# Performance work log

Hardware: AMD Instinct MI355X
Metric: run time of the kernel (lower is better)

The kernel has to match this reference:

```python
import jax, jax.numpy as jnp
import numpy as np

KH, KW = 3, 3
STRIDE = (1, 1)
PAD = (1, 1)
DIL = (1, 1)
DG = 1  # num_deformable_groups


def _out_size(h, pad, dil, k, stride):
    return (h + 2 * pad - (dil * (k - 1) + 1)) // stride + 1


def setup_inputs() -> dict:
    key = jax.random.key(0)
    k1, k2, k3 = jax.random.split(key, 3)
    B, Cin, H, W = 8, 128, 64, 64
    Cout = 128
    Ho = _out_size(H, PAD[0], DIL[0], KH, STRIDE[0])
    Wo = _out_size(W, PAD[1], DIL[1], KW, STRIDE[1])
    x = jax.random.normal(k1, (B, Cin, H, W), jnp.float32)
    offset = jax.random.normal(k2, (B, 2 * DG * KH * KW, Ho, Wo), jnp.float32)
    n = Cin * KH * KW
    stdv = 1.0 / np.sqrt(n)
    weight = jax.random.uniform(k3, (Cout, Cin, KH, KW), jnp.float32, -stdv, stdv)
    return {"x": x, "offset": offset, "weight": weight}


def deform_conv2d(x, offset, weight):
    B, Cin, H, W = x.shape
    Cout, _, kh, kw = weight.shape
    K = kh * kw
    Ho = _out_size(H, PAD[0], DIL[0], kh, STRIDE[0])
    Wo = _out_size(W, PAD[1], DIL[1], kw, STRIDE[1])
    G = DG
    Cg = Cin // G

    # base sampling grid per kernel tap: [kh,kw,Ho,Wo]
    by = (jnp.arange(kh) * DIL[0])[:, None, None, None] + (jnp.arange(Ho) * STRIDE[0] - PAD[0])[None, None, :, None]
    bx = (jnp.arange(kw) * DIL[1])[None, :, None, None] + (jnp.arange(Wo) * STRIDE[1] - PAD[1])[None, None, None, :]
    by = jnp.broadcast_to(by, (kh, kw, Ho, Wo)).reshape(K, Ho, Wo).astype(x.dtype)
    bx = jnp.broadcast_to(bx, (kh, kw, Ho, Wo)).reshape(K, Ho, Wo).astype(x.dtype)

    # offset layout: channel = g*2*K + 2*k + {0: dy, 1: dx}
    off = offset.reshape(B, G, K, 2, Ho, Wo)
    py = by[None, None] + off[:, :, :, 0]  # [B,G,K,Ho,Wo]
    px = bx[None, None] + off[:, :, :, 1]

    y0 = jnp.floor(py).astype(jnp.int32)
    x0 = jnp.floor(px).astype(jnp.int32)
    wy = (py - y0).reshape(B, G, 1, -1)  # fractional parts, [B,G,1,K*Ho*Wo]
    wx = (px - x0).reshape(B, G, 1, -1)

    xg = x.reshape(B, G, Cg, H * W)
    N = K * Ho * Wo

    def gather(yi, xi):
        valid = ((yi >= 0) & (yi < H) & (xi >= 0) & (xi < W)).reshape(B, G, 1, N)
        idx = (jnp.clip(yi, 0, H - 1) * W + jnp.clip(xi, 0, W - 1)).reshape(B, G, 1, N)
        v = jnp.take_along_axis(xg, jnp.broadcast_to(idx, (B, G, Cg, N)), axis=3)
        return v * valid.astype(x.dtype)

    v00 = gather(y0, x0)
    v01 = gather(y0, x0 + 1)
    v10 = gather(y0 + 1, x0)
    v11 = gather(y0 + 1, x0 + 1)

    cols = (v00 * (1 - wy) * (1 - wx) + v01 * (1 - wy) * wx
            + v10 * wy * (1 - wx) + v11 * wy * wx)
    cols = cols.reshape(B, G, Cg, K, Ho, Wo)  # deformable im2col columns

    wr = weight.reshape(Cout, G, Cg, K)
    return jnp.einsum('ogck,bgcknm->bonm', wr, cols)


def reference(x, offset, weight):
    return deform_conv2d(x, offset, weight)
```

## Files before the change

### kernel.cpp

```cpp
#include <hip/hip_runtime.h>
#include <hip/hip_fp16.h>

typedef __attribute__((ext_vector_type(4))) float f32x4;
typedef __attribute__((ext_vector_type(8))) _Float16 f16x8;
typedef __attribute__((ext_vector_type(4))) unsigned int u32x4;

__device__ __forceinline__ unsigned short f2h(float f) {
  __half h = __float2half_rn(f);
  unsigned short u;
  __builtin_memcpy(&u, &h, 2);
  return u;
}
__device__ __forceinline__ __half2 h2_of(unsigned int u) {
  __half2 h;
  __builtin_memcpy(&h, &u, 4);
  return h;
}
__device__ __forceinline__ unsigned int u_of(__half2 h) {
  unsigned int u;
  __builtin_memcpy(&u, &h, 4);
  return u;
}

__global__ __launch_bounds__(256) void xtrans_kernel(const float* __restrict__ x,
                                                     unsigned short* __restrict__ xt) {
  int t = blockIdx.x * 256 + threadIdx.x;
  int p  = t & 4095;
  int cg = (t >> 12) & 15;
  int b  = t >> 16;
  const float* xp = x + (((size_t)(b * 128 + cg * 8)) << 12) + p;
  unsigned int r[8];
#pragma unroll
  for (int j = 0; j < 8; ++j) r[j] = f2h(xp[(size_t)j << 12]);
  u32x4 pk;
  pk.x = r[0] | (r[1] << 16);
  pk.y = r[2] | (r[3] << 16);
  pk.z = r[4] | (r[5] << 16);
  pk.w = r[6] | (r[7] << 16);
  *reinterpret_cast<u32x4*>(xt + ((((size_t)b << 12) + p) << 7) + cg * 8) = pk;
}

__global__ __launch_bounds__(256) void wtrans_kernel(const float* __restrict__ w,
                                                     unsigned short* __restrict__ wf) {
  int tid = blockIdx.x * 256 + threadIdx.x;
  int l  = tid & 63;
  int mt = (tid >> 6) & 7;
  int ch = tid >> 9;
  int cc = ch / 9, tap = ch - cc * 9;
  int co = mt * 16 + (l & 15);
  int cb = cc * 32 + (l >> 4) * 8;
  unsigned int r[8];
#pragma unroll
  for (int j = 0; j < 8; ++j)
    r[j] = f2h(w[(co * 128 + cb + j) * 9 + tap]);
  u32x4 pk;
  pk.x = r[0] | (r[1] << 16);
  pk.y = r[2] | (r[3] << 16);
  pk.z = r[4] | (r[5] << 16);
  pk.w = r[6] | (r[7] << 16);
  *reinterpret_cast<u32x4*>(wf + (size_t)tid * 8) = pk;
}

__global__ __launch_bounds__(512, 1) void deform_kernel(const unsigned short* __restrict__ xt,
                                                        const float* __restrict__ off,
                                                        const unsigned short* __restrict__ wf,
                                                        float* __restrict__ out) {
  __shared__ __align__(16) unsigned char sWin[137216];
  __shared__ int   sPos[1152];
  __shared__ uint2 sWt[1152];

  const int tid = threadIdx.x;
  const int bid = blockIdx.x;
  const int b   = bid & 7;
  const int ho0 = (bid >> 3) * 2;
  const int r0  = min(max(ho0 - 3, 0), 56);

  for (int r = tid; r < 1152; r += 512) {
    int row = (r >= 576) ? 1 : 0;
    int rr  = r - row * 576;
    int tap = rr >> 6, wo = rr & 63;
    int ho = ho0 + row;
    float dy = off[((b * 18 + 2 * tap)     * 64 + ho) * 64 + wo];
    float dx = off[((b * 18 + 2 * tap + 1) * 64 + ho) * 64 + wo];
    float py = (float)(ho + (tap / 3) - 1) + dy;
    float px = (float)(wo + (tap % 3) - 1) + dx;
    float fy = floorf(py), fx = floorf(px);
    int y0 = (int)fy, x0 = (int)fx;
    float wy = py - fy, wx = px - fx;
    float wt = (y0 >= 0 && y0 < 64) ? (1.f - wy) : 0.f;
    float wb = (y0 + 1 >= 0 && y0 + 1 < 64) ? wy : 0.f;
    int y0c = min(max(y0, 0), 63), y1c = min(max(y0 + 1, 0), 63);
    int bx; float wl, wr;
    if (x0 >= 0 && x0 <= 62)      { bx = x0; wl = 1.f - wx; wr = wx;       }
    else if (x0 == -1)            { bx = 0;  wl = wx;       wr = 0.f;      }
    else if (x0 == 63)            { bx = 62; wl = 0.f;      wr = 1.f - wx; }
    else                          { bx = 0;  wl = 0.f;      wr = 0.f;      }
    sPos[r] = (y0c * 64 + bx) | ((y1c != y0c) ? (1 << 15) : 0);
    __half2 tp = __floats2half2_rn(wt * wl, wt * wr);
    __half2 bp = __floats2half2_rn(wb * wl, wb * wr);
    uint2 ww;
    ww.x = u_of(tp);
    ww.y = u_of(bp);
    sWt[r] = ww;
  }

  {
    const unsigned short* xrow = xt + ((size_t)b << 19) + ((size_t)r0 << 13);
#pragma unroll
    for (int it = 0; it < 16; ++it) {
      int idx = it * 512 + tid;
      int c = idx & 15;
      int p = (idx >> 4) & 63;
      int r = idx >> 10;
      u32x4 v;
      __builtin_memcpy(&v, xrow + (((size_t)(r * 64 + p)) << 7) + c * 8, 16);
      *reinterpret_cast<u32x4*>(&sWin[r * 16384 + p * 256 + (((c + p) & 15) << 4)]) = v;
    }
  }
  __syncthreads();

  const int l   = tid & 63;
  const int w   = tid >> 6;
  const int ks  = w & 3;
  const int row = w >> 2;
  const int ln  = l & 15;
  const int kg  = l >> 4;
  const int c16 = ks * 4 + kg;
  const int ho  = ho0 + row;

  const unsigned short* xtb = xt + ((size_t)b << 19) + ks * 32 + kg * 8;
  const unsigned short* wfb = wf + (size_t)l * 8;

  f32x4 acc[4][8] = {};

  for (int tap = 0; tap < 9; ++tap) {
    const int ch = ks * 9 + tap;

    f16x8 A[8];
    const unsigned short* wp = wfb + (size_t)(ch * 8) * 512;
#pragma unroll
    for (int mt = 0; mt < 8; ++mt)
      A[mt] = *reinterpret_cast<const f16x8*>(wp + (size_t)mt * 512);

#pragma unroll
    for (int pg = 0; pg < 4; ++pg) {
      const int e = row * 576 + tap * 64 + pg * 16 + ln;
      const int   pp = sPos[e];
      const uint2 ww = sWt[e];

      const int aX = pp & 4095;
      const int aY = aX + ((pp >> 9) & 64);
      const int tx  = aX & 63;
      const int twr = (aX >> 6) - r0;
      const int bwr = (aY >> 6) - r0;
      const bool tin = (unsigned)twr < 8u;
      const bool bin = (unsigned)bwr < 8u;

      u32x4 T0, T1, B0, B1;
      {
        int cT0 = ((c16 + tx) & 15) << 4, cT1 = ((c16 + tx + 1) & 15) << 4;
        int baseT = (tin ? twr : 0) * 16384 + tx * 256;
        __builtin_memcpy(&T0, &sWin[baseT + cT0],       16);
        __builtin_memcpy(&T1, &sWin[baseT + 256 + cT1], 16);
        int baseB = (bin ? bwr : 0) * 16384 + tx * 256;
        __builtin_memcpy(&B0, &sWin[baseB + cT0],       16);
        __builtin_memcpy(&B1, &sWin[baseB + 256 + cT1], 16);
      }
      if (!tin) {
        const unsigned short* p0 = xtb + ((size_t)aX << 7);
        __builtin_memcpy(&T0, p0,       16);
        __builtin_memcpy(&T1, p0 + 128, 16);
      }
      if (!bin) {
        const unsigned short* p1 = xtb + ((size_t)aY << 7);
        __builtin_memcpy(&B0, p1,       16);
        __builtin_memcpy(&B1, p1 + 128, 16);
      }

      const __half2 wtl = __half2half2(__low2half(h2_of(ww.x)));
      const __half2 wtr = __half2half2(__high2half(h2_of(ww.x)));
      const __half2 wbl = __half2half2(__low2half(h2_of(ww.y)));
      const __half2 wbr = __half2half2(__high2half(h2_of(ww.y)));
      u32x4 pk;
#pragma unroll
      for (int d = 0; d < 4; ++d) {
        __half2 s = __hmul2(wtl, h2_of(T0[d]));
        s = __hfma2(wtr, h2_of(T1[d]), s);
        s = __hfma2(wbl, h2_of(B0[d]), s);
        s = __hfma2(wbr, h2_of(B1[d]), s);
        pk[d] = u_of(s);
      }
      f16x8 bfrag;
      __builtin_memcpy(&bfrag, &pk, 16);

#pragma unroll
      for (int mt = 0; mt < 8; ++mt)
        acc[pg][mt] = __builtin_amdgcn_mfma_f32_16x16x32_f16(A[mt], bfrag,
                                                             acc[pg][mt], 0, 0, 0);
    }
  }

  float* sF = reinterpret_cast<float*>(sWin);
#define WR_LDS                                                                 \
  { _Pragma("unroll") for (int pg = 0; pg < 4; ++pg)                           \
    _Pragma("unroll") for (int mt = 0; mt < 8; ++mt)                           \
      *reinterpret_cast<f32x4*>(&sF[row * 8448 + (pg * 16 + ln) * 132 + mt * 16 + kg * 4]) = acc[pg][mt]; }
#define RD_LDS                                                                 \
  { _Pragma("unroll") for (int pg = 0; pg < 4; ++pg)                           \
    _Pragma("unroll") for (int mt = 0; mt < 8; ++mt) {                         \
      f32x4 v = *reinterpret_cast<const f32x4*>(&sF[row * 8448 + (pg * 16 + ln) * 132 + mt * 16 + kg * 4]); \
      acc[pg][mt] += v; } }

  __syncthreads();
  if (ks == 1) WR_LDS
  __syncthreads();
  if (ks == 0) RD_LDS
  __syncthreads();
  if (ks == 3) WR_LDS
  __syncthreads();
  if (ks == 2) RD_LDS
  __syncthreads();
  if (ks == 2) WR_LDS
  __syncthreads();
  if (ks == 0) RD_LDS
#undef WR_LDS
#undef RD_LDS

  {
    const int b2 = 16896 + row * 8704;
    if (ks == 0) {
#pragma unroll
      for (int pg = 0; pg < 4; ++pg)
#pragma unroll
        for (int mt = 0; mt < 8; ++mt)
#pragma unroll
          for (int rg = 0; rg < 4; ++rg)
            sF[b2 + (mt * 16 + kg * 4 + rg) * 68 + pg * 16 + ln] = acc[pg][mt][rg];
    }
    __syncthreads();
    if (ks == 0) {
      const int q4  = l & 15;
      const int ch2 = l >> 4;
      float* ob = out + (((size_t)b * 128) * 64 + ho) * 64 + q4 * 4;
#pragma unroll
      for (int i = 0; i < 32; ++i) {
        int co = ch2 * 32 + i;
        f32x4 v = *reinterpret_cast<const f32x4*>(&sF[b2 + co * 68 + q4 * 4]);
        *reinterpret_cast<f32x4*>(ob + (size_t)co * 4096) = v;
      }
    }
  }
}

extern "C" void kernel_launch(void* const* d_in, const int* in_sizes, int n_in,
                              void* d_out, int out_size, void* d_ws, size_t ws_size,
                              hipStream_t stream) {
  (void)in_sizes; (void)n_in; (void)out_size; (void)ws_size;
  const float* x   = (const float*)d_in[0];
  const float* off = (const float*)d_in[1];
  const float* w   = (const float*)d_in[2];
  float* out = (float*)d_out;
  unsigned short* xt = (unsigned short*)d_ws;
  unsigned short* wf = (unsigned short*)d_ws + (8388608 / 2);

  xtrans_kernel<<<2048, 256, 0, stream>>>(x, xt);
  wtrans_kernel<<<72, 256, 0, stream>>>(w, wf);
  deform_kernel<<<256, 512, 0, stream>>>(xt, off, wf, out);
}
```

Before: 102.5 us.

## Merge prep kernels, issue window loads early, parallelize split-K LDS reduction

The x-transpose and weight-pack kernels are merged into one launch using a block-index branch, which removes one kernel launch and its inter-kernel gap. The shared-memory window load is moved ahead of the offset/weight computation so its global loads overlap that arithmetic. The split-K reduction now writes two partial sums into separate LDS regions at once, cutting the reduction from six barrier phases to four. The final transpose buffer moves to offset 0, and correctness depends on the LDS regions not overlapping.

```diff
diff --git a/kernel.cpp b/kernel.cpp
--- a/kernel.cpp
+++ b/kernel.cpp
@@ -22,43 +22,44 @@
   return u;
 }
 
-__global__ __launch_bounds__(256) void xtrans_kernel(const float* __restrict__ x,
-                                                     unsigned short* __restrict__ xt) {
-  int t = blockIdx.x * 256 + threadIdx.x;
-  int p  = t & 4095;
-  int cg = (t >> 12) & 15;
-  int b  = t >> 16;
-  const float* xp = x + (((size_t)(b * 128 + cg * 8)) << 12) + p;
-  unsigned int r[8];
-#pragma unroll
-  for (int j = 0; j < 8; ++j) r[j] = f2h(xp[(size_t)j << 12]);
-  u32x4 pk;
-  pk.x = r[0] | (r[1] << 16);
-  pk.y = r[2] | (r[3] << 16);
-  pk.z = r[4] | (r[5] << 16);
-  pk.w = r[6] | (r[7] << 16);
-  *reinterpret_cast<u32x4*>(xt + ((((size_t)b << 12) + p) << 7) + cg * 8) = pk;
-}
-
-__global__ __launch_bounds__(256) void wtrans_kernel(const float* __restrict__ w,
-                                                     unsigned short* __restrict__ wf) {
-  int tid = blockIdx.x * 256 + threadIdx.x;
-  int l  = tid & 63;
-  int mt = (tid >> 6) & 7;
-  int ch = tid >> 9;
-  int cc = ch / 9, tap = ch - cc * 9;
-  int co = mt * 16 + (l & 15);
-  int cb = cc * 32 + (l >> 4) * 8;
-  unsigned int r[8];
-#pragma unroll
-  for (int j = 0; j < 8; ++j)
-    r[j] = f2h(w[(co * 128 + cb + j) * 9 + tap]);
-  u32x4 pk;
-  pk.x = r[0] | (r[1] << 16);
-  pk.y = r[2] | (r[3] << 16);
-  pk.z = r[4] | (r[5] << 16);
-  pk.w = r[6] | (r[7] << 16);
-  *reinterpret_cast<u32x4*>(wf + (size_t)tid * 8) = pk;
+__global__ __launch_bounds__(256) void prep_kernel(const float* __restrict__ x,
+                                                   const float* __restrict__ w,
+                                                   unsigned short* __restrict__ xt,
+                                                   unsigned short* __restrict__ wf) {
+  if (blockIdx.x < 2048) {
+    int t = blockIdx.x * 256 + threadIdx.x;
+    int p  = t & 4095;
+    int cg = (t >> 12) & 15;
+    int b  = t >> 16;
+    const float* xp = x + (((size_t)(b * 128 + cg * 8)) << 12) + p;
+    unsigned int r[8];
+#pragma unroll
+    for (int j = 0; j < 8; ++j) r[j] = f2h(xp[(size_t)j << 12]);
+    u32x4 pk;
+    pk.x = r[0] | (r[1] << 16);
+    pk.y = r[2] | (r[3] << 16);
+    pk.z = r[4] | (r[5] << 16);
+    pk.w = r[6] | (r[7] << 16);
+    *reinterpret_cast<u32x4*>(xt + ((((size_t)b << 12) + p) << 7) + cg * 8) = pk;
+  } else {
+    int tid = (blockIdx.x - 2048) * 256 + threadIdx.x;
+    int l  = tid & 63;
+    int mt = (tid >> 6) & 7;
+    int ch = tid >> 9;
+    int cc = ch / 9, tap = ch - cc * 9;
+    int co = mt * 16 + (l & 15);
+    int cb = cc * 32 + (l >> 4) * 8;
+    unsigned int r[8];
+#pragma unroll
+    for (int j = 0; j < 8; ++j)
+      r[j] = f2h(w[(co * 128 + cb + j) * 9 + tap]);
+    u32x4 pk;
+    pk.x = r[0] | (r[1] << 16);
+    pk.y = r[2] | (r[3] << 16);
+    pk.z = r[4] | (r[5] << 16);
+    pk.w = r[6] | (r[7] << 16);
+    *reinterpret_cast<u32x4*>(wf + (size_t)tid * 8) = pk;
+  }
 }
 
 __global__ __launch_bounds__(512, 1) void deform_kernel(const unsigned short* __restrict__ xt,
@@ -74,6 +75,20 @@
   const int b   = bid & 7;
   const int ho0 = (bid >> 3) * 2;
   const int r0  = min(max(ho0 - 3, 0), 56);
+
+  {
+    const unsigned short* xrow = xt + ((size_t)b << 19) + ((size_t)r0 << 13);
+#pragma unroll
+    for (int it = 0; it < 16; ++it) {
+      int idx = it * 512 + tid;
+      int c = idx & 15;
+      int p = (idx >> 4) & 63;
+      int r = idx >> 10;
+      u32x4 v;
+      __builtin_memcpy(&v, xrow + (((size_t)(r * 64 + p)) << 7) + c * 8, 16);
+      *reinterpret_cast<u32x4*>(&sWin[r * 16384 + p * 256 + (((c + p) & 15) << 4)]) = v;
+    }
+  }
 
   for (int r = tid; r < 1152; r += 512) {
     int row = (r >= 576) ? 1 : 0;
@@ -103,20 +118,6 @@
     ww.y = u_of(bp);
     sWt[r] = ww;
   }
-
-  {
-    const unsigned short* xrow = xt + ((size_t)b << 19) + ((size_t)r0 << 13);
-#pragma unroll
-    for (int it = 0; it < 16; ++it) {
-      int idx = it * 512 + tid;
-      int c = idx & 15;
-      int p = (idx >> 4) & 63;
-      int r = idx >> 10;
-      u32x4 v;
-      __builtin_memcpy(&v, xrow + (((size_t)(r * 64 + p)) << 7) + c * 8, 16);
-      *reinterpret_cast<u32x4*>(&sWin[r * 16384 + p * 256 + (((c + p) & 15) << 4)]) = v;
-    }
-  }
   __syncthreads();
 
   const int l   = tid & 63;
@@ -201,33 +202,31 @@
   }
 
   float* sF = reinterpret_cast<float*>(sWin);
-#define WR_LDS                                                                 \
+#define WR_LDS(BASE)                                                           \
   { _Pragma("unroll") for (int pg = 0; pg < 4; ++pg)                           \
     _Pragma("unroll") for (int mt = 0; mt < 8; ++mt)                           \
-      *reinterpret_cast<f32x4*>(&sF[row * 8448 + (pg * 16 + ln) * 132 + mt * 16 + kg * 4]) = acc[pg][mt]; }
-#define RD_LDS                                                                 \
+      *reinterpret_cast<f32x4*>(&sF[(BASE) + row * 8448 + (pg * 16 + ln) * 132 + mt * 16 + kg * 4]) = acc[pg][mt]; }
+#define RD_LDS(BASE)                                                           \
   { _Pragma("unroll") for (int pg = 0; pg < 4; ++pg)                           \
     _Pragma("unroll") for (int mt = 0; mt < 8; ++mt) {                         \
-      f32x4 v = *reinterpret_cast<const f32x4*>(&sF[row * 8448 + (pg * 16 + ln) * 132 + mt * 16 + kg * 4]); \
+      f32x4 v = *reinterpret_cast<const f32x4*>(&sF[(BASE) + row * 8448 + (pg * 16 + ln) * 132 + mt * 16 + kg * 4]); \
       acc[pg][mt] += v; } }
 
   __syncthreads();
-  if (ks == 1) WR_LDS
-  __syncthreads();
-  if (ks == 0) RD_LDS
-  __syncthreads();
-  if (ks == 3) WR_LDS
-  __syncthreads();
-  if (ks == 2) RD_LDS
-  __syncthreads();
-  if (ks == 2) WR_LDS
-  __syncthreads();
-  if (ks == 0) RD_LDS
+  if (ks == 1) WR_LDS(17408)
+  if (ks == 3) WR_LDS(0)
+  __syncthreads();
+  if (ks == 0) RD_LDS(17408)
+  if (ks == 2) RD_LDS(0)
+  __syncthreads();
+  if (ks == 2) WR_LDS(17408)
+  __syncthreads();
+  if (ks == 0) RD_LDS(17408)
 #undef WR_LDS
 #undef RD_LDS
 
   {
-    const int b2 = 16896 + row * 8704;
+    const int b2 = row * 8704;
     if (ks == 0) {
 #pragma unroll
       for (int pg = 0; pg < 4; ++pg)
@@ -263,7 +262,6 @@
   unsigned short* xt = (unsigned short*)d_ws;
   unsigned short* wf = (unsigned short*)d_ws + (8388608 / 2);
 
-  xtrans_kernel<<<2048, 256, 0, stream>>>(x, xt);
-  wtrans_kernel<<<72, 256, 0, stream>>>(w, wf);
+  prep_kernel<<<2120, 256, 0, stream>>>(x, w, xt, wf);
   deform_kernel<<<256, 512, 0, stream>>>(xt, off, wf, out);
 }
```

Result: no change. 100.8 us (-1.7%).
